# Performance work log

Hardware: AMD Instinct MI355X
Metric: run time of the kernel (lower is better)

Reference implementation:

```python
import jax, jax.numpy as jnp
import numpy as np

DIM_MODEL = 1024
NUM_HEADS = 16
DROPOUT_P = 0.5
SCALE = float(np.sqrt(DIM_MODEL // NUM_HEADS))  # NOTE: source MULTIPLIES by this (unusual but faithful)
DROP_KEY = jax.random.key(42)


def setup_inputs() -> dict:
    key = jax.random.key(0)
    ks = jax.random.split(key, 9)
    B, LQ, LK, D = 4, 2048, 2048, DIM_MODEL
    s = 1.0 / np.sqrt(D)
    return {
        "query": jax.random.normal(ks[0], (B, LQ, D), jnp.float32),
        "key": jax.random.normal(ks[1], (B, LK, D), jnp.float32),
        "value": jax.random.normal(ks[2], (B, LK, D), jnp.float32),
        "Wq": jax.random.normal(ks[3], (D, D), jnp.float32) * s,
        "bq": jax.random.normal(ks[4], (D,), jnp.float32) * s,
        "Wk": jax.random.normal(ks[5], (D, D), jnp.float32) * s,
        "bk": jax.random.normal(ks[6], (D,), jnp.float32) * s,
        "Wv": jax.random.normal(ks[7], (D, D), jnp.float32) * s,
        "bv": jax.random.normal(ks[8], (D,), jnp.float32) * s,
    }


def reference(query, key, value, Wq, bq, Wk, bk, Wv, bv):
    # Linear projections (W stored as [in, out])
    q = jnp.einsum('bqd,de->bqe', query, Wq) + bq
    k = jnp.einsum('bkd,de->bke', key, Wk) + bk
    v = jnp.einsum('bkd,de->bke', value, Wv) + bv
    # scores scaled by MULTIPLYING sqrt(d_head), per source
    scores = jnp.einsum('bqe,bke->bqk', q, k) * SCALE
    probs = jax.nn.softmax(scores, axis=-1)
    # dropout (train mode, p=0.5), deterministic fixed key for reproducibility
    keep = jax.random.bernoulli(DROP_KEY, 1.0 - DROPOUT_P, probs.shape)
    probs = jnp.where(keep, probs / (1.0 - DROPOUT_P), 0.0)
    return jnp.einsum('bqk,bke->bqe', probs, v)
```

## Files before the change

### kernel.cpp

```cpp
#include <hip/hip_runtime.h>
#include <math.h>

#define BATCH  4
#define LSEQ   2048
#define DMODEL 1024
#define MROWS  (BATCH * LSEQ)
#define SCORE_SCALE 8.0f

#define THREEFRY_PARTITIONABLE 1

typedef __bf16 bf16_t;
typedef bf16_t bf16x8 __attribute__((ext_vector_type(8)));
typedef bf16_t bf16x4 __attribute__((ext_vector_type(4)));
typedef float  f32x4  __attribute__((ext_vector_type(4)));

#define LDSP(p) ((__attribute__((address_space(3))) void*)(p))
#define GLBP(p) ((const __attribute__((address_space(1))) void*)(p))

__device__ __forceinline__ unsigned rotl32(unsigned x, int r) {
    return (x << r) | (x >> (32 - r));
}

__device__ __forceinline__ void threefry2x32(unsigned k0, unsigned k1,
                                             unsigned x0, unsigned x1,
                                             unsigned& o0, unsigned& o1) {
    const unsigned ks0 = k0, ks1 = k1, ks2 = k0 ^ k1 ^ 0x1BD11BDAu;
    x0 += ks0; x1 += ks1;
#define TF_R(r) { x0 += x1; x1 = rotl32(x1, r); x1 ^= x0; }
    TF_R(13) TF_R(15) TF_R(26) TF_R(6)
    x0 += ks1; x1 += ks2 + 1u;
    TF_R(17) TF_R(29) TF_R(16) TF_R(24)
    x0 += ks2; x1 += ks0 + 2u;
    TF_R(13) TF_R(15) TF_R(26) TF_R(6)
    x0 += ks0; x1 += ks1 + 3u;
    TF_R(17) TF_R(29) TF_R(16) TF_R(24)
    x0 += ks1; x1 += ks2 + 4u;
    TF_R(13) TF_R(15) TF_R(26) TF_R(6)
    x0 += ks2; x1 += ks0 + 5u;
#undef TF_R
    o0 = x0; o1 = x1;
}

__device__ __forceinline__ bool dropout_keep(unsigned n) {
    unsigned o0, o1;
#if THREEFRY_PARTITIONABLE
    threefry2x32(0u, 42u, 0u, n, o0, o1);
    unsigned bits = o0 ^ o1;
#else
    const unsigned HALF = (unsigned)(BATCH * LSEQ) * (unsigned)LSEQ / 2u;
    unsigned c0 = (n < HALF) ? n : (n - HALF);
    unsigned c1 = (n < HALF) ? (n + HALF) : n;
    threefry2x32(0u, 42u, c0, c1, o0, o1);
    unsigned bits = (n < HALF) ? o0 : o1;
#endif
    return bits < 0x80000000u;
}

__global__ __launch_bounds__(256)
void split_f32(const float* __restrict__ X0, const float* __restrict__ X1,
               bf16_t* __restrict__ hi, bf16_t* __restrict__ lo, int n) {
    const int y = blockIdx.y;
    const float* X = y ? X1 : X0;
    long long i = (long long)(blockIdx.x * 256 + threadIdx.x) * 4;
    if (i >= n) return;
    float4 v = *(const float4*)(X + i);
    bf16x4 h, l;
    h[0] = (bf16_t)v.x; l[0] = (bf16_t)(v.x - (float)h[0]);
    h[1] = (bf16_t)v.y; l[1] = (bf16_t)(v.y - (float)h[1]);
    h[2] = (bf16_t)v.z; l[2] = (bf16_t)(v.z - (float)h[2]);
    h[3] = (bf16_t)v.w; l[3] = (bf16_t)(v.w - (float)h[3]);
    *(bf16x4*)(hi + (long long)y * n + i) = h;
    *(bf16x4*)(lo + (long long)y * n + i) = l;
}

__global__ __launch_bounds__(256)
void split_transpose(const float* __restrict__ W0, const float* __restrict__ W1,
                     bf16_t* __restrict__ Th, bf16_t* __restrict__ Tl,
                     int Kd, int Nd) {
    __shared__ float t[32][33];
    const int z = blockIdx.z;
    const float* W = z ? W1 : W0;
    const long long zo = (long long)z * Kd * Nd;
    const int bx = blockIdx.x * 32;
    const int by = blockIdx.y * 32;
    const int tx = threadIdx.x & 31, ty = threadIdx.x >> 5;
#pragma unroll
    for (int i = 0; i < 4; ++i)
        t[ty + i * 8][tx] = W[(long long)(by + ty + i * 8) * Nd + bx + tx];
    __syncthreads();
#pragma unroll
    for (int i = 0; i < 4; ++i) {
        float v = t[tx][ty + i * 8];
        long long idx = zo + (long long)(bx + ty + i * 8) * Kd + by + tx;
        bf16_t h = (bf16_t)v;
        Th[idx] = h;
        Tl[idx] = (bf16_t)(v - (float)h);
    }
}

template <int SPLIT, int OUT, int BROW>
__global__ __launch_bounds__(256)
void gemm_mfma(const bf16_t* __restrict__ Ah, const bf16_t* __restrict__ Al,
               const bf16_t* __restrict__ Bh, const bf16_t* __restrict__ Bl,
               const float* __restrict__ bias, const float* __restrict__ bias2,
               float* __restrict__ Cf, bf16_t* __restrict__ Ch,
               bf16_t* __restrict__ Cl,
               int M, int N, int K, float scale,
               long long sA, long long sB, long long sC) {
    constexpr int TM = 128, TN = 128, TOT = 256, CHUNKS = 4;
    constexpr int NB = SPLIT ? 2 : 1;
    constexpr int BUFSZ = NB * TOT * 32;
    __shared__ __align__(16) bf16_t smem[2 * BUFSZ];

    const int tid = threadIdx.x;
    const int lane = tid & 63;
    const int wave = tid >> 6;
    const int quad = lane >> 4;
    const int l16 = lane & 15;
    const int wm = (wave & 1) * 64;
    const int wn = (wave >> 1) * 64;
    const long long z = blockIdx.z;
    const int m0 = blockIdx.y * TM, n0 = blockIdx.x * TN;

    const bf16_t* gAh = Ah + z * sA;
    const bf16_t* gBh = Bh + z * sB;
    const bf16_t* gAl = SPLIT ? Al + z * sA : nullptr;
    const bf16_t* gBl = SPLIT ? Bl + z * sB : nullptr;

    const int lrow = lane >> 2;
    const int scol = ((lane & 3) ^ ((lrow >> 1) & 3)) * 8;
    const int sw = (l16 >> 1) & 3;

    auto issue = [&](int k0, int b) {
        bf16_t* base = smem + b * BUFSZ;
#pragma unroll
        for (int c = 0; c < CHUNKS; ++c) {
            const int rbase = wave * 64 + c * 16;
            const int row = rbase + lrow;
            if (rbase < TM) {
                const long long g = (long long)(m0 + row) * K + k0 + scol;
                __builtin_amdgcn_global_load_lds(GLBP(gAh + g), LDSP(base + row * 32), 16, 0, 0);
                if constexpr (SPLIT)
                    __builtin_amdgcn_global_load_lds(GLBP(gAl + g), LDSP(base + TOT * 32 + row * 32), 16, 0, 0);
            } else {
                const int br = row - TM;
                const long long g = (long long)(n0 + br) * K + k0 + scol;
                __builtin_amdgcn_global_load_lds(GLBP(gBh + g), LDSP(base + TM * 32 + br * 32), 16, 0, 0);
                if constexpr (SPLIT)
                    __builtin_amdgcn_global_load_lds(GLBP(gBl + g), LDSP(base + TOT * 32 + TM * 32 + br * 32), 16, 0, 0);
            }
        }
    };

    f32x4 acc[4][4];
#pragma unroll
    for (int i = 0; i < 4; ++i)
#pragma unroll
        for (int j = 0; j < 4; ++j)
            acc[i][j] = (f32x4){0.f, 0.f, 0.f, 0.f};

    issue(0, 0);
    const int NIT = K >> 5;
    for (int it = 0; it < NIT; ++it) {
        const int b = it & 1;
        const bool more = (it + 1) < NIT;
        if (more) issue((it + 1) << 5, b ^ 1);
        if constexpr (SPLIT) {
            if (more) asm volatile("s_waitcnt vmcnt(8)" ::: "memory");
            else      asm volatile("s_waitcnt vmcnt(0)" ::: "memory");
        } else {
            if (more) asm volatile("s_waitcnt vmcnt(4)" ::: "memory");
            else      asm volatile("s_waitcnt vmcnt(0)" ::: "memory");
        }
        asm volatile("s_barrier" ::: "memory");

        bf16_t* base = smem + b * BUFSZ;
        bf16_t* sAh = base;
        bf16_t* sBh = base + TM * 32;
        bf16_t* sAl = base + TOT * 32;
        bf16_t* sBl = base + TOT * 32 + TM * 32;

        bf16x8 afh[4], bfh[4], afl[4], bfl[4];
#pragma unroll
        for (int i = 0; i < 4; ++i) {
            const int ao = (wm + i * 16 + l16) * 32 + (quad ^ sw) * 8;
            afh[i] = *(const bf16x8*)(sAh + ao);
            if constexpr (SPLIT) afl[i] = *(const bf16x8*)(sAl + ao);
        }
#pragma unroll
        for (int j = 0; j < 4; ++j) {
            const int bo = (wn + j * 16 + l16) * 32 + (quad ^ sw) * 8;
            bfh[j] = *(const bf16x8*)(sBh + bo);
            if constexpr (SPLIT) bfl[j] = *(const bf16x8*)(sBl + bo);
        }
#pragma unroll
        for (int i = 0; i < 4; ++i)
#pragma unroll
            for (int j = 0; j < 4; ++j) {
                acc[i][j] = __builtin_amdgcn_mfma_f32_16x16x32_bf16(afh[i], bfh[j], acc[i][j], 0, 0, 0);
                if constexpr (SPLIT) {
                    acc[i][j] = __builtin_amdgcn_mfma_f32_16x16x32_bf16(afh[i], bfl[j], acc[i][j], 0, 0, 0);
                    acc[i][j] = __builtin_amdgcn_mfma_f32_16x16x32_bf16(afl[i], bfh[j], acc[i][j], 0, 0, 0);
                }
            }
        asm volatile("s_barrier" ::: "memory");
    }

    const float* bz = (z == 1 && bias2) ? bias2 : bias;
#pragma unroll
    for (int i = 0; i < 4; ++i)
#pragma unroll
        for (int j = 0; j < 4; ++j) {
            const int n = n0 + wn + j * 16 + l16;
            float bvn = 0.f;
            if constexpr (OUT != 0 && !BROW) bvn = bz[n];
#pragma unroll
            for (int r = 0; r < 4; ++r) {
                const int m = m0 + wm + i * 16 + quad * 4 + r;
                const long long idx = z * sC + (long long)m * N + n;
                float v = acc[i][j][r];
                if constexpr (OUT == 0) {
                    Cf[idx] = v * scale;
                } else if constexpr (OUT == 1) {
                    v += bvn;
                    bf16_t h = (bf16_t)v;
                    Ch[idx] = h;
                    Cl[idx] = (bf16_t)(v - (float)h);
                } else {
                    v += BROW ? bz[m] : bvn;
                    Ch[idx] = (bf16_t)v;
                }
            }
        }
}

__global__ __launch_bounds__(256)
void softmax_dropout(const float* __restrict__ S, bf16_t* __restrict__ P) {
    const int LK = LSEQ;
    const unsigned row = blockIdx.x;
    const float* rowp = S + (long long)row * LK;
    bf16_t* prow = P + (long long)row * LK;
    __shared__ float buf[LSEQ];
    __shared__ float rbuf[256];
    const int tid = threadIdx.x;

    float m = -INFINITY;
    for (int j = tid; j < LK; j += 256) {
        float v = rowp[j];
        buf[j] = v;
        m = fmaxf(m, v);
    }
    rbuf[tid] = m;
    __syncthreads();
    for (int s = 128; s > 0; s >>= 1) {
        if (tid < s) rbuf[tid] = fmaxf(rbuf[tid], rbuf[tid + s]);
        __syncthreads();
    }
    m = rbuf[0];
    __syncthreads();

    float l = 0.f;
    for (int j = tid; j < LK; j += 256) {
        float e = expf(buf[j] - m);
        buf[j] = e;
        l += e;
    }
    rbuf[tid] = l;
    __syncthreads();
    for (int s = 128; s > 0; s >>= 1) {
        if (tid < s) rbuf[tid] += rbuf[tid + s];
        __syncthreads();
    }
    l = rbuf[0];

    const float inv = 2.0f / l;
    for (int j = tid; j < LK; j += 256) {
        unsigned n = row * (unsigned)LK + (unsigned)j;
        float p = dropout_keep(n) ? buf[j] * inv : 0.0f;
        prow[j] = (bf16_t)p;
    }
}

extern "C" void kernel_launch(void* const* d_in, const int* in_sizes, int n_in,
                              void* d_out, int out_size, void* d_ws, size_t ws_size,
                              hipStream_t stream) {
    const float* query = (const float*)d_in[0];
    const float* key_  = (const float*)d_in[1];
    const float* value = (const float*)d_in[2];
    const float* Wq = (const float*)d_in[3];
    const float* bq = (const float*)d_in[4];
    const float* Wk = (const float*)d_in[5];
    const float* bk = (const float*)d_in[6];
    const float* Wv = (const float*)d_in[7];
    const float* bv = (const float*)d_in[8];
    float* out = (float*)d_out;

    char* w = (char*)d_ws;
    const size_t Q1 = (size_t)MROWS * DMODEL * 2;
    bf16_t* Qh  = (bf16_t*)(w);
    bf16_t* Ql  = (bf16_t*)(w + 2 * Q1);
    bf16_t* VT  = (bf16_t*)(w + 4 * Q1);
    float*  S   = (float*)(w + 5 * Q1);
    bf16_t* XvH  = (bf16_t*)(w + 5 * Q1);
    bf16_t* XvL  = (bf16_t*)(w + 6 * Q1);
    bf16_t* XqkH = (bf16_t*)(w + 5 * Q1);
    bf16_t* XqkL = (bf16_t*)(w + 7 * Q1);
    bf16_t* WTh = (bf16_t*)(w + 9 * Q1);
    bf16_t* WTl = (bf16_t*)(w + 9 * Q1 + 2 * (size_t)DMODEL * DMODEL * 2);
    bf16_t* P   = Qh;

    dim3 b256(256);
    const int NELEM = MROWS * DMODEL;
    const long long DD = (long long)DMODEL * DMODEL;
    dim3 gwt1(DMODEL / 32, DMODEL / 32, 1);
    dim3 gwt2(DMODEL / 32, DMODEL / 32, 2);

    split_transpose<<<gwt1, b256, 0, stream>>>(Wv, nullptr, WTh, WTl, DMODEL, DMODEL);
    split_f32<<<dim3(NELEM / 1024, 1), b256, 0, stream>>>(value, nullptr, XvH, XvL, NELEM);
    gemm_mfma<0, 2, 1><<<dim3(LSEQ / 128, DMODEL / 128, BATCH), b256, 0, stream>>>(
        WTh, nullptr, XvH, nullptr, bv, nullptr, nullptr, VT, nullptr,
        DMODEL, LSEQ, DMODEL, 1.f,
        0, (long long)LSEQ * DMODEL, (long long)DMODEL * LSEQ);

    split_transpose<<<gwt2, b256, 0, stream>>>(Wq, Wk, WTh, WTl, DMODEL, DMODEL);
    split_f32<<<dim3(NELEM / 1024, 2), b256, 0, stream>>>(query, key_, XqkH, XqkL, NELEM);
    gemm_mfma<1, 1, 0><<<dim3(DMODEL / 128, MROWS / 128, 2), b256, 0, stream>>>(
        XqkH, XqkL, WTh, WTl, bq, bk, nullptr, Qh, Ql,
        MROWS, DMODEL, DMODEL, 1.f,
        (long long)NELEM, DD, (long long)NELEM);

    gemm_mfma<1, 0, 0><<<dim3(LSEQ / 128, LSEQ / 128, BATCH), b256, 0, stream>>>(
        Qh, Ql, Qh + NELEM, Ql + NELEM, nullptr, nullptr, S, nullptr, nullptr,
        LSEQ, LSEQ, DMODEL, SCORE_SCALE,
        (long long)LSEQ * DMODEL, (long long)LSEQ * DMODEL,
        (long long)LSEQ * LSEQ);

    softmax_dropout<<<dim3(MROWS), b256, 0, stream>>>(S, P);

    gemm_mfma<0, 0, 0><<<dim3(DMODEL / 128, LSEQ / 128, BATCH), b256, 0, stream>>>(
        P, nullptr, VT, nullptr, nullptr, nullptr, out, nullptr, nullptr,
        LSEQ, DMODEL, LSEQ, 1.f,
        (long long)LSEQ * LSEQ, (long long)DMODEL * LSEQ,
        (long long)LSEQ * DMODEL);
}
```

Baseline: 502.6 us.

## Switch GEMM to 32x32 MFMA with B operand loaded directly to registers

Rewrites the GEMM inner loop to use 32x32x16 bf16 MFMA instructions. Only the A tile is staged in LDS; the B fragments are loaded straight from global memory into registers, which halves LDS traffic and shared memory per block. A launch-bounds occupancy hint is added. The softmax is rewritten to hold each row's eight values per thread in registers with wave-shuffle reductions, and the value input now gets a plain bf16 conversion instead of a hi/lo split. Loading B directly from global memory risks uncoalesced, higher-latency loads.

```diff
diff --git a/kernel.cpp b/kernel.cpp
--- a/kernel.cpp
+++ b/kernel.cpp
@@ -12,7 +12,7 @@
 typedef __bf16 bf16_t;
 typedef bf16_t bf16x8 __attribute__((ext_vector_type(8)));
 typedef bf16_t bf16x4 __attribute__((ext_vector_type(4)));
-typedef float  f32x4  __attribute__((ext_vector_type(4)));
+typedef float  f32x16 __attribute__((ext_vector_type(16)));
 
 #define LDSP(p) ((__attribute__((address_space(3))) void*)(p))
 #define GLBP(p) ((const __attribute__((address_space(1))) void*)(p))
@@ -74,6 +74,18 @@
 }
 
 __global__ __launch_bounds__(256)
+void cvt_bf16(const float* __restrict__ X, bf16_t* __restrict__ Y, int n) {
+    long long i = (long long)(blockIdx.x * 256 + threadIdx.x) * 8;
+    if (i >= n) return;
+    float4 a = *(const float4*)(X + i);
+    float4 b = *(const float4*)(X + i + 4);
+    bf16x8 o;
+    o[0] = (bf16_t)a.x; o[1] = (bf16_t)a.y; o[2] = (bf16_t)a.z; o[3] = (bf16_t)a.w;
+    o[4] = (bf16_t)b.x; o[5] = (bf16_t)b.y; o[6] = (bf16_t)b.z; o[7] = (bf16_t)b.w;
+    *(bf16x8*)(Y + i) = o;
+}
+
+__global__ __launch_bounds__(256)
 void split_transpose(const float* __restrict__ W0, const float* __restrict__ W1,
                      bf16_t* __restrict__ Th, bf16_t* __restrict__ Tl,
                      int Kd, int Nd) {
@@ -99,7 +111,7 @@
 }
 
 template <int SPLIT, int OUT, int BROW>
-__global__ __launch_bounds__(256)
+__global__ __launch_bounds__(256, 3)
 void gemm_mfma(const bf16_t* __restrict__ Ah, const bf16_t* __restrict__ Al,
                const bf16_t* __restrict__ Bh, const bf16_t* __restrict__ Bl,
                const float* __restrict__ bias, const float* __restrict__ bias2,
@@ -107,118 +119,124 @@
                bf16_t* __restrict__ Cl,
                int M, int N, int K, float scale,
                long long sA, long long sB, long long sC) {
-    constexpr int TM = 128, TN = 128, TOT = 256, CHUNKS = 4;
-    constexpr int NB = SPLIT ? 2 : 1;
-    constexpr int BUFSZ = NB * TOT * 32;
+    constexpr int PL = 128 * 32;
+    constexpr int NP = SPLIT ? 2 : 1;
+    constexpr int BUFSZ = NP * PL;
     __shared__ __align__(16) bf16_t smem[2 * BUFSZ];
 
     const int tid = threadIdx.x;
     const int lane = tid & 63;
     const int wave = tid >> 6;
-    const int quad = lane >> 4;
-    const int l16 = lane & 15;
+    const int l32 = lane & 31;
+    const int ksel = lane >> 5;
     const int wm = (wave & 1) * 64;
     const int wn = (wave >> 1) * 64;
     const long long z = blockIdx.z;
-    const int m0 = blockIdx.y * TM, n0 = blockIdx.x * TN;
+    const int m0 = blockIdx.y * 128, n0 = blockIdx.x * 128;
 
     const bf16_t* gAh = Ah + z * sA;
+    const bf16_t* gAl = SPLIT ? Al + z * sA : nullptr;
     const bf16_t* gBh = Bh + z * sB;
-    const bf16_t* gAl = SPLIT ? Al + z * sA : nullptr;
     const bf16_t* gBl = SPLIT ? Bl + z * sB : nullptr;
 
     const int lrow = lane >> 2;
-    const int scol = ((lane & 3) ^ ((lrow >> 1) & 3)) * 8;
-    const int sw = (l16 >> 1) & 3;
-
-    auto issue = [&](int k0, int b) {
+    const int sgrp = ((lane & 3) ^ ((lrow >> 1) & 3)) * 8;
+
+    const bf16_t* pBh[2];
+    const bf16_t* pBl[2];
+#pragma unroll
+    for (int j = 0; j < 2; ++j) {
+        const long long nn = (long long)(n0 + wn + j * 32 + l32) * K + ksel * 8;
+        pBh[j] = gBh + nn;
+        if constexpr (SPLIT) pBl[j] = gBl + nn;
+    }
+
+    auto issueA = [&](int k0, int b) {
         bf16_t* base = smem + b * BUFSZ;
 #pragma unroll
-        for (int c = 0; c < CHUNKS; ++c) {
-            const int rbase = wave * 64 + c * 16;
-            const int row = rbase + lrow;
-            if (rbase < TM) {
-                const long long g = (long long)(m0 + row) * K + k0 + scol;
-                __builtin_amdgcn_global_load_lds(GLBP(gAh + g), LDSP(base + row * 32), 16, 0, 0);
-                if constexpr (SPLIT)
-                    __builtin_amdgcn_global_load_lds(GLBP(gAl + g), LDSP(base + TOT * 32 + row * 32), 16, 0, 0);
-            } else {
-                const int br = row - TM;
-                const long long g = (long long)(n0 + br) * K + k0 + scol;
-                __builtin_amdgcn_global_load_lds(GLBP(gBh + g), LDSP(base + TM * 32 + br * 32), 16, 0, 0);
-                if constexpr (SPLIT)
-                    __builtin_amdgcn_global_load_lds(GLBP(gBl + g), LDSP(base + TOT * 32 + TM * 32 + br * 32), 16, 0, 0);
-            }
+        for (int c = 0; c < 2; ++c) {
+            const int row = wave * 32 + c * 16 + lrow;
+            const long long g = (long long)(m0 + row) * K + k0 + sgrp;
+            __builtin_amdgcn_global_load_lds(GLBP(gAh + g), LDSP(base + row * 32), 16, 0, 0);
+            if constexpr (SPLIT)
+                __builtin_amdgcn_global_load_lds(GLBP(gAl + g), LDSP(base + PL + row * 32), 16, 0, 0);
         }
     };
 
-    f32x4 acc[4][4];
-#pragma unroll
-    for (int i = 0; i < 4; ++i)
-#pragma unroll
-        for (int j = 0; j < 4; ++j)
-            acc[i][j] = (f32x4){0.f, 0.f, 0.f, 0.f};
-
-    issue(0, 0);
+    f32x16 acc[2][2];
+#pragma unroll
+    for (int i = 0; i < 2; ++i)
+#pragma unroll
+        for (int j = 0; j < 2; ++j)
+#pragma unroll
+            for (int r = 0; r < 16; ++r) acc[i][j][r] = 0.f;
+
+    bf16x8 bh[2][2], bl[2][2];
+
+    issueA(0, 0);
     const int NIT = K >> 5;
     for (int it = 0; it < NIT; ++it) {
         const int b = it & 1;
         const bool more = (it + 1) < NIT;
-        if (more) issue((it + 1) << 5, b ^ 1);
+        const int k0 = it << 5;
+#pragma unroll
+        for (int j = 0; j < 2; ++j)
+#pragma unroll
+            for (int kh = 0; kh < 2; ++kh) {
+                bh[j][kh] = *(const bf16x8*)(pBh[j] + k0 + kh * 16);
+                if constexpr (SPLIT) bl[j][kh] = *(const bf16x8*)(pBl[j] + k0 + kh * 16);
+            }
+        if (more) issueA(k0 + 32, b ^ 1);
         if constexpr (SPLIT) {
-            if (more) asm volatile("s_waitcnt vmcnt(8)" ::: "memory");
-            else      asm volatile("s_waitcnt vmcnt(0)" ::: "memory");
+            if (more) asm volatile("s_waitcnt vmcnt(12)" ::: "memory");
+            else      asm volatile("s_waitcnt vmcnt(8)" ::: "memory");
         } else {
-            if (more) asm volatile("s_waitcnt vmcnt(4)" ::: "memory");
-            else      asm volatile("s_waitcnt vmcnt(0)" ::: "memory");
+            if (more) asm volatile("s_waitcnt vmcnt(6)" ::: "memory");
+            else      asm volatile("s_waitcnt vmcnt(4)" ::: "memory");
         }
         asm volatile("s_barrier" ::: "memory");
 
         bf16_t* base = smem + b * BUFSZ;
-        bf16_t* sAh = base;
-        bf16_t* sBh = base + TM * 32;
-        bf16_t* sAl = base + TOT * 32;
-        bf16_t* sBl = base + TOT * 32 + TM * 32;
-
-        bf16x8 afh[4], bfh[4], afl[4], bfl[4];
-#pragma unroll
-        for (int i = 0; i < 4; ++i) {
-            const int ao = (wm + i * 16 + l16) * 32 + (quad ^ sw) * 8;
-            afh[i] = *(const bf16x8*)(sAh + ao);
-            if constexpr (SPLIT) afl[i] = *(const bf16x8*)(sAl + ao);
-        }
-#pragma unroll
-        for (int j = 0; j < 4; ++j) {
-            const int bo = (wn + j * 16 + l16) * 32 + (quad ^ sw) * 8;
-            bfh[j] = *(const bf16x8*)(sBh + bo);
-            if constexpr (SPLIT) bfl[j] = *(const bf16x8*)(sBl + bo);
-        }
-#pragma unroll
-        for (int i = 0; i < 4; ++i)
-#pragma unroll
-            for (int j = 0; j < 4; ++j) {
-                acc[i][j] = __builtin_amdgcn_mfma_f32_16x16x32_bf16(afh[i], bfh[j], acc[i][j], 0, 0, 0);
-                if constexpr (SPLIT) {
-                    acc[i][j] = __builtin_amdgcn_mfma_f32_16x16x32_bf16(afh[i], bfl[j], acc[i][j], 0, 0, 0);
-                    acc[i][j] = __builtin_amdgcn_mfma_f32_16x16x32_bf16(afl[i], bfh[j], acc[i][j], 0, 0, 0);
+        const int sw = (l32 >> 1) & 3;
+        bf16x8 ah[2][2], al[2][2];
+#pragma unroll
+        for (int i = 0; i < 2; ++i)
+#pragma unroll
+            for (int kh = 0; kh < 2; ++kh) {
+                const int r = wm + i * 32 + l32;
+                const int g = ((kh * 2 + ksel) ^ sw) * 8;
+                ah[i][kh] = *(const bf16x8*)(base + r * 32 + g);
+                if constexpr (SPLIT) al[i][kh] = *(const bf16x8*)(base + PL + r * 32 + g);
+            }
+#pragma unroll
+        for (int kh = 0; kh < 2; ++kh)
+#pragma unroll
+            for (int i = 0; i < 2; ++i)
+#pragma unroll
+                for (int j = 0; j < 2; ++j) {
+                    acc[i][j] = __builtin_amdgcn_mfma_f32_32x32x16_bf16(ah[i][kh], bh[j][kh], acc[i][j], 0, 0, 0);
+                    if constexpr (SPLIT) {
+                        acc[i][j] = __builtin_amdgcn_mfma_f32_32x32x16_bf16(ah[i][kh], bl[j][kh], acc[i][j], 0, 0, 0);
+                        acc[i][j] = __builtin_amdgcn_mfma_f32_32x32x16_bf16(al[i][kh], bh[j][kh], acc[i][j], 0, 0, 0);
+                    }
                 }
-            }
         asm volatile("s_barrier" ::: "memory");
     }
 
     const float* bz = (z == 1 && bias2) ? bias2 : bias;
 #pragma unroll
-    for (int i = 0; i < 4; ++i)
-#pragma unroll
-        for (int j = 0; j < 4; ++j) {
-            const int n = n0 + wn + j * 16 + l16;
+    for (int i = 0; i < 2; ++i)
+#pragma unroll
+        for (int j = 0; j < 2; ++j) {
+            const int n = n0 + wn + j * 32 + l32;
             float bvn = 0.f;
             if constexpr (OUT != 0 && !BROW) bvn = bz[n];
 #pragma unroll
-            for (int r = 0; r < 4; ++r) {
-                const int m = m0 + wm + i * 16 + quad * 4 + r;
+            for (int reg = 0; reg < 16; ++reg) {
+                const int rr = (reg & 3) + 8 * (reg >> 2) + 4 * ksel;
+                const int m = m0 + wm + i * 32 + rr;
                 const long long idx = z * sC + (long long)m * N + n;
-                float v = acc[i][j][r];
+                float v = acc[i][j][reg];
                 if constexpr (OUT == 0) {
                     Cf[idx] = v * scale;
                 } else if constexpr (OUT == 1) {
@@ -236,49 +254,41 @@
 
 __global__ __launch_bounds__(256)
 void softmax_dropout(const float* __restrict__ S, bf16_t* __restrict__ P) {
-    const int LK = LSEQ;
     const unsigned row = blockIdx.x;
-    const float* rowp = S + (long long)row * LK;
-    bf16_t* prow = P + (long long)row * LK;
-    __shared__ float buf[LSEQ];
-    __shared__ float rbuf[256];
+    const float* rp = S + (long long)row * LSEQ;
     const int tid = threadIdx.x;
 
-    float m = -INFINITY;
-    for (int j = tid; j < LK; j += 256) {
-        float v = rowp[j];
-        buf[j] = v;
-        m = fmaxf(m, v);
-    }
-    rbuf[tid] = m;
+    float v[8];
+    *(float4*)(v)     = *(const float4*)(rp + tid * 8);
+    *(float4*)(v + 4) = *(const float4*)(rp + tid * 8 + 4);
+
+    float m = v[0];
+#pragma unroll
+    for (int e = 1; e < 8; ++e) m = fmaxf(m, v[e]);
+#pragma unroll
+    for (int o = 1; o < 64; o <<= 1) m = fmaxf(m, __shfl_xor(m, o));
+    __shared__ float redm[4];
+    if ((tid & 63) == 0) redm[tid >> 6] = m;
     __syncthreads();
-    for (int s = 128; s > 0; s >>= 1) {
-        if (tid < s) rbuf[tid] = fmaxf(rbuf[tid], rbuf[tid + s]);
-        __syncthreads();
-    }
-    m = rbuf[0];
+    m = fmaxf(fmaxf(redm[0], redm[1]), fmaxf(redm[2], redm[3]));
+
+    float s = 0.f;
+#pragma unroll
+    for (int e = 0; e < 8; ++e) { v[e] = __expf(v[e] - m); s += v[e]; }
+#pragma unroll
+    for (int o = 1; o < 64; o <<= 1) s += __shfl_xor(s, o);
+    __shared__ float reds[4];
+    if ((tid & 63) == 0) reds[tid >> 6] = s;
     __syncthreads();
-
-    float l = 0.f;
-    for (int j = tid; j < LK; j += 256) {
-        float e = expf(buf[j] - m);
-        buf[j] = e;
-        l += e;
-    }
-    rbuf[tid] = l;
-    __syncthreads();
-    for (int s = 128; s > 0; s >>= 1) {
-        if (tid < s) rbuf[tid] += rbuf[tid + s];
-        __syncthreads();
-    }
-    l = rbuf[0];
-
-    const float inv = 2.0f / l;
-    for (int j = tid; j < LK; j += 256) {
-        unsigned n = row * (unsigned)LK + (unsigned)j;
-        float p = dropout_keep(n) ? buf[j] * inv : 0.0f;
-        prow[j] = (bf16_t)p;
-    }
+    s = (reds[0] + reds[1]) + (reds[2] + reds[3]);
+
+    const float inv = 2.0f / s;
+    const unsigned nb = row * (unsigned)LSEQ + (unsigned)(tid * 8);
+    bf16x8 o8;
+#pragma unroll
+    for (int e = 0; e < 8; ++e)
+        o8[e] = (bf16_t)(dropout_keep(nb + e) ? v[e] * inv : 0.0f);
+    *(bf16x8*)(P + (long long)row * LSEQ + tid * 8) = o8;
 }
 
 extern "C" void kernel_launch(void* const* d_in, const int* in_sizes, int n_in,
@@ -302,7 +312,6 @@
     bf16_t* VT  = (bf16_t*)(w + 4 * Q1);
     float*  S   = (float*)(w + 5 * Q1);
     bf16_t* XvH  = (bf16_t*)(w + 5 * Q1);
-    bf16_t* XvL  = (bf16_t*)(w + 6 * Q1);
     bf16_t* XqkH = (bf16_t*)(w + 5 * Q1);
     bf16_t* XqkL = (bf16_t*)(w + 7 * Q1);
     bf16_t* WTh = (bf16_t*)(w + 9 * Q1);
@@ -316,7 +325,7 @@
     dim3 gwt2(DMODEL / 32, DMODEL / 32, 2);
 
     split_transpose<<<gwt1, b256, 0, stream>>>(Wv, nullptr, WTh, WTl, DMODEL, DMODEL);
-    split_f32<<<dim3(NELEM / 1024, 1), b256, 0, stream>>>(value, nullptr, XvH, XvL, NELEM);
+    cvt_bf16<<<dim3(NELEM / 2048), b256, 0, stream>>>(value, XvH, NELEM);
     gemm_mfma<0, 2, 1><<<dim3(LSEQ / 128, DMODEL / 128, BATCH), b256, 0, stream>>>(
         WTh, nullptr, XvH, nullptr, bv, nullptr, nullptr, VT, nullptr,
         DMODEL, LSEQ, DMODEL, 1.f,
```

New measurement: 635.5 us. 1.26x slower.
